# Kernel tuning notes

Hardware: AMD Instinct MI355X
Metric: run time of the kernel (lower is better)

Reference implementation:

```python
import jax, jax.numpy as jnp
import numpy as np

HEAD_SIZE = 16  # matches init_kwargs head_size


def _rope_angles(seq_len, half_dim, base=10000.0):
    # standard RoPE frequencies, matches typical precompute_pos_cis
    freqs = 1.0 / (base ** (np.arange(0, half_dim, dtype=np.float32) / half_dim))
    t = np.arange(seq_len, dtype=np.float32)
    ang = np.outer(t, freqs)  # (S, half_dim)
    return jnp.asarray(np.cos(ang)), jnp.asarray(np.sin(ang))


def setup_inputs() -> dict:
    key = jax.random.key(0)
    ks = jax.random.split(key, 10)
    B, S, D = 2, 2048, 1024
    hd = D // HEAD_SIZE
    pos_cos, pos_sin = _rope_angles(S, hd // 2)
    w = lambda k: jax.random.normal(k, (D, D), jnp.float32) * 0.02
    b = lambda k: jax.random.normal(k, (D,), jnp.float32) * 0.02
    return {
        "x": jax.random.normal(ks[0], (B, S, D), jnp.float32),
        "pos_cos": pos_cos,
        "pos_sin": pos_sin,
        "wq_w": w(ks[1]), "wq_b": b(ks[2]),
        "wk_w": w(ks[3]), "wk_b": b(ks[4]),
        "wv_w": w(ks[5]), "wv_b": b(ks[6]),
        "wo_w": w(ks[7]), "wo_b": b(ks[8]),
    }


def _apply_rope(t, cos, sin):
    # t: (B, S, H, hd); cos/sin: (S, hd//2) -> broadcast (1, S, 1, hd//2)
    B, S, H, hd = t.shape
    tr = t.reshape(B, S, H, hd // 2, 2)
    a, b = tr[..., 0], tr[..., 1]
    c = cos[None, :, None, :]
    s = sin[None, :, None, :]
    # complex multiply (a + ib) * (c + is)
    out_r = a * c - b * s
    out_i = a * s + b * c
    return jnp.stack([out_r, out_i], axis=-1).reshape(B, S, H, hd)


def reference(x, pos_cos, pos_sin, wq_w, wq_b, wk_w, wk_b, wv_w, wv_b, wo_w, wo_b):
    B, S, D = x.shape
    H = HEAD_SIZE
    hd = D // H
    q = (x @ wq_w.T + wq_b).reshape(B, S, H, hd)
    k = (x @ wk_w.T + wk_b).reshape(B, S, H, hd)
    v = (x @ wv_w.T + wv_b).reshape(B, S, H, hd)
    q = _apply_rope(q, pos_cos, pos_sin)
    k = _apply_rope(k, pos_cos, pos_sin)
    scale = 1.0 / jnp.sqrt(jnp.asarray(hd, x.dtype))
    scores = jnp.einsum('bshd,bthd->bhst', q, k) * scale  # (B,H,S,S)
    causal = jnp.tril(jnp.ones((S, S), bool))
    scores = jnp.where(causal[None, None], scores, jnp.asarray(-jnp.inf, scores.dtype))
    probs = jax.nn.softmax(scores, axis=-1)
    out = jnp.einsum('bhst,bthd->bshd', probs, v).reshape(B, S, D)
    return out @ wo_w.T + wo_b
```

## Files before the change

### kernel.cpp

```cpp
#include <hip/hip_runtime.h>
#include <stdint.h>
#include <stddef.h>


typedef __bf16 bf16x8 __attribute__((ext_vector_type(8)));
typedef float  f32x4  __attribute__((ext_vector_type(4)));

__device__ __forceinline__ unsigned short f2b(float f) {
  union { float f; uint32_t u; } v; v.f = f;
  uint32_t u = v.u;
  return (unsigned short)((u + 0x7FFFu + ((u >> 16) & 1u)) >> 16);
}

__device__ __forceinline__ void async16(const void* g, void* l) {
  __builtin_amdgcn_global_load_lds(
      (const __attribute__((address_space(1))) void*)g,
      (__attribute__((address_space(3))) void*)l, 16, 0, 0);
}

__global__ void cast_kernel(const float* __restrict__ in,
                            unsigned short* __restrict__ out, int n4) {
  int i = blockIdx.x * blockDim.x + threadIdx.x;
  if (i >= n4) return;
  float4 v = ((const float4*)in)[i];
  ushort4 o;
  o.x = f2b(v.x); o.y = f2b(v.y); o.z = f2b(v.z); o.w = f2b(v.w);
  ((ushort4*)out)[i] = o;
}

__global__ void cast_w_kernel(const float* __restrict__ wq, const float* __restrict__ wk,
                              const float* __restrict__ wv, const float* __restrict__ wo,
                              unsigned short* __restrict__ wqkv,
                              unsigned short* __restrict__ wobf) {
  int i = blockIdx.x * blockDim.x + threadIdx.x;
  const int sel = i >> 18, k = i & ((1 << 18) - 1);
  const float* src = (sel == 0) ? wq : (sel == 1) ? wk : (sel == 2) ? wv : wo;
  float4 v = ((const float4*)src)[k];
  ushort4 o;
  o.x = f2b(v.x); o.y = f2b(v.y); o.z = f2b(v.z); o.w = f2b(v.w);
  if (sel < 3) ((ushort4*)wqkv)[(size_t)sel * 262144 + k] = o;
  else         ((ushort4*)wobf)[k] = o;
}

__global__ __launch_bounds__(256) void qkv_gemm_kernel(
    const unsigned short* __restrict__ A,
    const unsigned short* __restrict__ W,
    const float* __restrict__ biasq, const float* __restrict__ biask,
    const float* __restrict__ biasv,
    const float* __restrict__ cp, const float* __restrict__ sp,
    unsigned short* __restrict__ qo,
    unsigned short* __restrict__ ko,
    unsigned short* __restrict__ vo)
{
  __shared__ unsigned short As[128 * 64];
  __shared__ unsigned short Bs[128 * 64];
  const int tid  = threadIdx.x;
  const int w    = tid >> 6, l = tid & 63;
  const int lm   = l & 15,  quad = l >> 4;
  const int nblk = blockIdx.x;
  const int m0   = blockIdx.y * 128;
  const int n0g  = nblk * 128;
  const int wm   = (w >> 1) * 64, wn = (w & 1) * 64;

  const f32x4 fzero = {0.f, 0.f, 0.f, 0.f};
  f32x4 acc[4][4];
#pragma unroll
  for (int i = 0; i < 4; ++i)
#pragma unroll
    for (int j = 0; j < 4; ++j) acc[i][j] = fzero;

  for (int k0 = 0; k0 < 1024; k0 += 64) {
    __syncthreads();
#pragma unroll
    for (int q = 0; q < 4; ++q) {
      const int row = w * 16 + lm + (q & 1) * 64;
      const int kc  = quad + (q >> 1) * 4;
      const size_t ldsb = ((size_t)(w + 4 * (q & 1)) * 128 + 64 * (q >> 1)) * 8;
      async16(A + (size_t)(m0 + row) * 1024 + k0 + kc * 8, As + ldsb);
      async16(W + (size_t)(n0g + row) * 1024 + k0 + kc * 8, Bs + ldsb);
    }
    __syncthreads();
#pragma unroll
    for (int kk = 0; kk < 2; ++kk) {
      bf16x8 af[4], bfc[4];
#pragma unroll
      for (int i = 0; i < 4; ++i)
        af[i] = *(const bf16x8*)(As + (size_t)((((w >> 1) * 4 + i) * 128 + kk * 64 + l)) * 8);
#pragma unroll
      for (int j = 0; j < 4; ++j)
        bfc[j] = *(const bf16x8*)(Bs + (size_t)((((w & 1) * 4 + j) * 128 + kk * 64 + l)) * 8);
#pragma unroll
      for (int i = 0; i < 4; ++i)
#pragma unroll
        for (int j = 0; j < 4; ++j)
          acc[i][j] = __builtin_amdgcn_mfma_f32_16x16x32_bf16(af[i], bfc[j], acc[i][j], 0, 0, 0);
    }
  }

  const int which = nblk >> 3;
  const int n0    = (nblk & 7) * 128;
  const float* bias = (which == 0) ? biasq : (which == 1) ? biask : biasv;
#pragma unroll
  for (int i = 0; i < 4; ++i) {
#pragma unroll
    for (int j = 0; j < 4; ++j) {
      const int n = n0 + wn + j * 16 + lm;
      const float bval = bias[n];
      const int h = n >> 6, d = n & 63;
      float vals[4];
#pragma unroll
      for (int r = 0; r < 4; ++r) {
        const int m = m0 + wm + i * 16 + quad * 4 + r;
        const int srow = m & 2047;
        float val = acc[i][j][r] + bval;
        if (which != 2) {
          const float c  = cp[srow * 32 + (d >> 1)];
          const float sn = sp[srow * 32 + (d >> 1)];
          const float part = __shfl_xor(val, 1, 64);
          val = (d & 1) ? (part * sn + val * c) : (val * c - part * sn);
        }
        vals[r] = val;
      }
      const int mbase = m0 + wm + i * 16 + quad * 4;
      const int b = mbase >> 11, s0 = mbase & 2047;
      const int bh = (b << 4) + h;
      if (which == 0) {
#pragma unroll
        for (int r = 0; r < 4; ++r)
          qo[((size_t)bh * 2048 + s0 + r) * 64 + d] = f2b(vals[r]);
      } else if (which == 1) {
#pragma unroll
        for (int r = 0; r < 4; ++r) {
          const int s = s0 + r;
          ko[((size_t)bh * 32 + (s >> 6)) * 4096 +
             (size_t)(((d >> 3) * 64 + (s & 63))) * 8 + (d & 7)] = f2b(vals[r]);
        }
      } else {
        uint32_t w0 = (uint32_t)f2b(vals[0]) | ((uint32_t)f2b(vals[1]) << 16);
        uint32_t w1 = (uint32_t)f2b(vals[2]) | ((uint32_t)f2b(vals[3]) << 16);
        uint2 pk; pk.x = w0; pk.y = w1;
        *(uint2*)(vo + ((size_t)bh * 32 + (s0 >> 6)) * 4096 +
                  (size_t)((((s0 & 63) >> 3) * 64 + d)) * 8 + (s0 & 7)) = pk;
      }
    }
  }
}

__global__ __launch_bounds__(256, 4) void flash_kernel(
    const unsigned short* __restrict__ Q,
    const unsigned short* __restrict__ K,
    const unsigned short* __restrict__ VT,
    unsigned short* __restrict__ O)
{
  constexpr int PSTRIDE = 72;
  __shared__ unsigned short Ps[64 * PSTRIDE];
  const int tid = threadIdx.x;
  const int w = tid >> 6, l = tid & 63, lm = l & 15, quad = l >> 4;
  const int bh = blockIdx.x, qt = 31 - (int)blockIdx.y;
  const int row0 = qt * 64 + w * 16;

  bf16x8 aq[2];
#pragma unroll
  for (int kc = 0; kc < 2; ++kc)
    aq[kc] = *(const bf16x8*)(Q + ((size_t)bh * 2048 + row0 + lm) * 64 + kc * 32 + quad * 8);

  const f32x4 fzero = {0.f, 0.f, 0.f, 0.f};
  f32x4 Oacc[4];
#pragma unroll
  for (int jo = 0; jo < 4; ++jo) Oacc[jo] = fzero;
  float m_i = -1e30f, l_i = 0.f;

  const int nkv = qt + 1;

#pragma unroll 1
  for (int kt = 0; kt < nkv - 1; ++kt) {
    const size_t tbase = ((size_t)bh * 32 + kt) * 4096;
    bf16x8 kf[2][4], vf[2][4];
#pragma unroll
    for (int kc = 0; kc < 2; ++kc)
#pragma unroll
      for (int tb = 0; tb < 4; ++tb) {
        const size_t off = tbase + (size_t)(((kc * 4 + quad) * 64 + tb * 16 + lm)) * 8;
        kf[kc][tb] = *(const bf16x8*)(K + off);
        vf[kc][tb] = *(const bf16x8*)(VT + off);
      }
    f32x4 Sc[4];
#pragma unroll
    for (int tb = 0; tb < 4; ++tb) Sc[tb] = fzero;
#pragma unroll
    for (int kc = 0; kc < 2; ++kc)
#pragma unroll
      for (int tb = 0; tb < 4; ++tb)
        Sc[tb] = __builtin_amdgcn_mfma_f32_16x16x32_bf16(kf[kc][tb], aq[kc], Sc[tb], 0, 0, 0);

    float mx = -1e30f;
#pragma unroll
    for (int tb = 0; tb < 4; ++tb)
#pragma unroll
      for (int r = 0; r < 4; ++r) {
        float s = Sc[tb][r] * 0.125f;
        Sc[tb][r] = s;
        mx = fmaxf(mx, s);
      }
    mx = fmaxf(mx, __shfl_xor(mx, 16, 64));
    mx = fmaxf(mx, __shfl_xor(mx, 32, 64));

    const bool skip = (bool)__all(mx - m_i <= 8.0f);
    float alpha = 1.f;
    if (!skip) {
      const float mnew = fmaxf(m_i, mx);
      alpha = __expf(m_i - mnew);
      m_i = mnew;
    }
    const float mref = m_i;

    float ps = 0.f;
#pragma unroll
    for (int tb = 0; tb < 4; ++tb) {
      float p0 = __expf(Sc[tb][0] - mref), p1 = __expf(Sc[tb][1] - mref);
      float p2 = __expf(Sc[tb][2] - mref), p3 = __expf(Sc[tb][3] - mref);
      ps += (p0 + p1) + (p2 + p3);
      uint2 pk;
      pk.x = (uint32_t)f2b(p0) | ((uint32_t)f2b(p1) << 16);
      pk.y = (uint32_t)f2b(p2) | ((uint32_t)f2b(p3) << 16);
      *(uint2*)(Ps + (size_t)(w * 16 + lm) * PSTRIDE + tb * 16 + quad * 4) = pk;
    }
    ps += __shfl_xor(ps, 16, 64);
    ps += __shfl_xor(ps, 32, 64);
    if (skip) {
      l_i += ps;
    } else {
      l_i = l_i * alpha + ps;
      float af4[4];
#pragma unroll
      for (int r = 0; r < 4; ++r) af4[r] = __shfl(alpha, quad * 4 + r, 64);
#pragma unroll
      for (int jo = 0; jo < 4; ++jo)
#pragma unroll
        for (int r = 0; r < 4; ++r) Oacc[jo][r] *= af4[r];
    }

#pragma unroll
    for (int kc = 0; kc < 2; ++kc) {
      bf16x8 ap = *(const bf16x8*)(Ps + (size_t)(w * 16 + lm) * PSTRIDE + kc * 32 + quad * 8);
#pragma unroll
      for (int jo = 0; jo < 4; ++jo)
        Oacc[jo] = __builtin_amdgcn_mfma_f32_16x16x32_bf16(ap, vf[kc][jo], Oacc[jo], 0, 0, 0);
    }
  }

  {
    const size_t tbase = ((size_t)bh * 32 + qt) * 4096;
    bf16x8 kf[2][4], vf[2][4];
#pragma unroll
    for (int kc = 0; kc < 2; ++kc)
#pragma unroll
      for (int tb = 0; tb < 4; ++tb) {
        const size_t off = tbase + (size_t)(((kc * 4 + quad) * 64 + tb * 16 + lm)) * 8;
        kf[kc][tb] = *(const bf16x8*)(K + off);
        vf[kc][tb] = *(const bf16x8*)(VT + off);
      }
    f32x4 Sc[4];
#pragma unroll
    for (int tb = 0; tb < 4; ++tb) Sc[tb] = fzero;
#pragma unroll
    for (int kc = 0; kc < 2; ++kc)
#pragma unroll
      for (int tb = 0; tb < 4; ++tb)
        Sc[tb] = __builtin_amdgcn_mfma_f32_16x16x32_bf16(kf[kc][tb], aq[kc], Sc[tb], 0, 0, 0);

    const int mrel = w * 16 + lm;
    float mx = -1e30f;
#pragma unroll
    for (int tb = 0; tb < 4; ++tb)
#pragma unroll
      for (int r = 0; r < 4; ++r) {
        float s = Sc[tb][r] * 0.125f;
        if (tb * 16 + quad * 4 + r > mrel) s = -1e30f;
        Sc[tb][r] = s;
        mx = fmaxf(mx, s);
      }
    mx = fmaxf(mx, __shfl_xor(mx, 16, 64));
    mx = fmaxf(mx, __shfl_xor(mx, 32, 64));
    const float mnew  = fmaxf(m_i, mx);
    const float alpha = __expf(m_i - mnew);
    m_i = mnew;

    float ps = 0.f;
#pragma unroll
    for (int tb = 0; tb < 4; ++tb) {
      float p0 = __expf(Sc[tb][0] - mnew), p1 = __expf(Sc[tb][1] - mnew);
      float p2 = __expf(Sc[tb][2] - mnew), p3 = __expf(Sc[tb][3] - mnew);
      ps += (p0 + p1) + (p2 + p3);
      uint2 pk;
      pk.x = (uint32_t)f2b(p0) | ((uint32_t)f2b(p1) << 16);
      pk.y = (uint32_t)f2b(p2) | ((uint32_t)f2b(p3) << 16);
      *(uint2*)(Ps + (size_t)(w * 16 + lm) * PSTRIDE + tb * 16 + quad * 4) = pk;
    }
    ps += __shfl_xor(ps, 16, 64);
    ps += __shfl_xor(ps, 32, 64);
    l_i = l_i * alpha + ps;

    float af4[4];
#pragma unroll
    for (int r = 0; r < 4; ++r) af4[r] = __shfl(alpha, quad * 4 + r, 64);
#pragma unroll
    for (int jo = 0; jo < 4; ++jo)
#pragma unroll
      for (int r = 0; r < 4; ++r) Oacc[jo][r] *= af4[r];

#pragma unroll
    for (int kc = 0; kc < 2; ++kc) {
      bf16x8 ap = *(const bf16x8*)(Ps + (size_t)(w * 16 + lm) * PSTRIDE + kc * 32 + quad * 8);
#pragma unroll
      for (int jo = 0; jo < 4; ++jo)
        Oacc[jo] = __builtin_amdgcn_mfma_f32_16x16x32_bf16(ap, vf[kc][jo], Oacc[jo], 0, 0, 0);
    }
  }

  float lf[4];
#pragma unroll
  for (int r = 0; r < 4; ++r) lf[r] = 1.0f / __shfl(l_i, quad * 4 + r, 64);
  const int b = bh >> 4, h = bh & 15;
#pragma unroll
  for (int jo = 0; jo < 4; ++jo)
#pragma unroll
    for (int r = 0; r < 4; ++r) {
      const int s   = row0 + quad * 4 + r;
      const int col = h * 64 + jo * 16 + lm;
      O[((size_t)b * 2048 + s) * 1024 + col] = f2b(Oacc[jo][r] * lf[r]);
    }
}

__global__ __launch_bounds__(256) void oproj_gemm_kernel(
    const unsigned short* __restrict__ A,
    const unsigned short* __restrict__ W,
    const float* __restrict__ bias,
    float* __restrict__ out)
{
  __shared__ unsigned short As[64 * 64];
  __shared__ unsigned short Bs[128 * 64];
  const int tid = threadIdx.x;
  const int w = tid >> 6, l = tid & 63;
  const int lm = l & 15, quad = l >> 4;
  const int m0 = blockIdx.y * 64;
  const int n0 = blockIdx.x * 128;

  const f32x4 fzero = {0.f, 0.f, 0.f, 0.f};
  f32x4 acc[4][2];
#pragma unroll
  for (int i = 0; i < 4; ++i)
#pragma unroll
    for (int j = 0; j < 2; ++j) acc[i][j] = fzero;

  for (int k0 = 0; k0 < 1024; k0 += 64) {
    __syncthreads();
#pragma unroll
    for (int q = 0; q < 2; ++q) {
      const int row = w * 16 + lm;
      const int kc  = quad + 4 * q;
      async16(A + (size_t)(m0 + row) * 1024 + k0 + kc * 8,
              As + ((size_t)w * 128 + 64 * q) * 8);
    }
#pragma unroll
    for (int q = 0; q < 4; ++q) {
      const int row = w * 16 + lm + (q & 1) * 64;
      const int kc  = quad + 4 * (q >> 1);
      async16(W + (size_t)(n0 + row) * 1024 + k0 + kc * 8,
              Bs + ((size_t)(w + 4 * (q & 1)) * 128 + 64 * (q >> 1)) * 8);
    }
    __syncthreads();
#pragma unroll
    for (int kk = 0; kk < 2; ++kk) {
      bf16x8 af[4], bfc[2];
#pragma unroll
      for (int i = 0; i < 4; ++i)
        af[i] = *(const bf16x8*)(As + (size_t)((i * 128 + kk * 64 + l)) * 8);
#pragma unroll
      for (int j = 0; j < 2; ++j)
        bfc[j] = *(const bf16x8*)(Bs + (size_t)(((w * 2 + j) * 128 + kk * 64 + l)) * 8);
#pragma unroll
      for (int i = 0; i < 4; ++i)
#pragma unroll
        for (int j = 0; j < 2; ++j)
          acc[i][j] = __builtin_amdgcn_mfma_f32_16x16x32_bf16(af[i], bfc[j], acc[i][j], 0, 0, 0);
    }
  }

#pragma unroll
  for (int i = 0; i < 4; ++i) {
#pragma unroll
    for (int j = 0; j < 2; ++j) {
      const int n = n0 + w * 32 + j * 16 + lm;
      const float bval = bias[n];
#pragma unroll
      for (int r = 0; r < 4; ++r) {
        const int m = m0 + i * 16 + quad * 4 + r;
        out[(size_t)m * 1024 + n] = acc[i][j][r] + bval;
      }
    }
  }
}

extern "C" void kernel_launch(void* const* d_in, const int* in_sizes, int n_in,
                              void* d_out, int out_size, void* d_ws, size_t ws_size,
                              hipStream_t stream) {
  (void)in_sizes; (void)n_in; (void)out_size; (void)ws_size;
  const float* x  = (const float*)d_in[0];
  const float* cp = (const float*)d_in[1];
  const float* sp = (const float*)d_in[2];
  const float* wq = (const float*)d_in[3];
  const float* bq = (const float*)d_in[4];
  const float* wk = (const float*)d_in[5];
  const float* bk = (const float*)d_in[6];
  const float* wv = (const float*)d_in[7];
  const float* bv = (const float*)d_in[8];
  const float* wo = (const float*)d_in[9];
  const float* bo = (const float*)d_in[10];
  float* out = (float*)d_out;

  unsigned short* xbf  = (unsigned short*)d_ws;
  unsigned short* wqkv = xbf  + (size_t)4 * 1024 * 1024;
  unsigned short* wobf = wqkv + (size_t)3 * 1024 * 1024;
  unsigned short* qbf  = wobf + (size_t)1 * 1024 * 1024;
  unsigned short* kbf  = qbf  + (size_t)4 * 1024 * 1024;
  unsigned short* vbf  = kbf  + (size_t)4 * 1024 * 1024;
  unsigned short* obf  = vbf  + (size_t)4 * 1024 * 1024;

  hipLaunchKernelGGL(cast_kernel, dim3(4096), dim3(256), 0, stream, x, xbf, 1048576);
  hipLaunchKernelGGL(cast_w_kernel, dim3(4096), dim3(256), 0, stream,
                     wq, wk, wv, wo, wqkv, wobf);

  hipLaunchKernelGGL(qkv_gemm_kernel, dim3(24, 32), dim3(256), 0, stream,
                     xbf, wqkv, bq, bk, bv, cp, sp, qbf, kbf, vbf);
  hipLaunchKernelGGL(flash_kernel, dim3(32, 32), dim3(256), 0, stream,
                     qbf, kbf, vbf, obf);
  hipLaunchKernelGGL(oproj_gemm_kernel, dim3(8, 64), dim3(256), 0, stream,
                     obf, wobf, bo, out);
}
```

Baseline: 226.7 us.

## Pre-tile QKV GEMM operands in cast kernels and read fragments directly from global

```diff
diff --git a/kernel.cpp b/kernel.cpp
--- a/kernel.cpp
+++ b/kernel.cpp
@@ -16,6 +16,47 @@
   __builtin_amdgcn_global_load_lds(
       (const __attribute__((address_space(1))) void*)g,
       (__attribute__((address_space(3))) void*)l, 16, 0, 0);
+}
+
+__global__ void cast_x_tiled_kernel(const float* __restrict__ in,
+                                    unsigned short* __restrict__ out) {
+  int i = blockIdx.x * blockDim.x + threadIdx.x;
+  const int L  = i & 1023;
+  const int kt = (i >> 10) & 15;
+  const int pn = i >> 14;
+  const int row = pn * 128 + ((L >> 7) << 4) + (L & 15);
+  const int k0  = kt * 64 + ((L >> 4) & 7) * 8;
+  const float4* src = (const float4*)(in + (size_t)row * 1024 + k0);
+  float4 a = src[0], b = src[1];
+  uint4 pk;
+  pk.x = (uint32_t)f2b(a.x) | ((uint32_t)f2b(a.y) << 16);
+  pk.y = (uint32_t)f2b(a.z) | ((uint32_t)f2b(a.w) << 16);
+  pk.z = (uint32_t)f2b(b.x) | ((uint32_t)f2b(b.y) << 16);
+  pk.w = (uint32_t)f2b(b.z) | ((uint32_t)f2b(b.w) << 16);
+  *(uint4*)(out + (size_t)i * 8) = pk;
+}
+
+__global__ void cast_w_tiled_kernel(const float* __restrict__ wq,
+                                    const float* __restrict__ wk,
+                                    const float* __restrict__ wv,
+                                    unsigned short* __restrict__ out) {
+  int i = blockIdx.x * blockDim.x + threadIdx.x;
+  const int mat = i >> 17;
+  const int rem = i & 131071;
+  const int L  = rem & 1023;
+  const int kt = (rem >> 10) & 15;
+  const int pn = rem >> 14;
+  const float* src = (mat == 0) ? wq : (mat == 1) ? wk : wv;
+  const int row = pn * 128 + ((L >> 7) << 4) + (L & 15);
+  const int k0  = kt * 64 + ((L >> 4) & 7) * 8;
+  const float4* s = (const float4*)(src + (size_t)row * 1024 + k0);
+  float4 a = s[0], b = s[1];
+  uint4 pk;
+  pk.x = (uint32_t)f2b(a.x) | ((uint32_t)f2b(a.y) << 16);
+  pk.y = (uint32_t)f2b(a.z) | ((uint32_t)f2b(a.w) << 16);
+  pk.z = (uint32_t)f2b(b.x) | ((uint32_t)f2b(b.y) << 16);
+  pk.w = (uint32_t)f2b(b.z) | ((uint32_t)f2b(b.w) << 16);
+  *(uint4*)(out + (size_t)i * 8) = pk;
 }
 
 __global__ void cast_kernel(const float* __restrict__ in,
@@ -28,21 +69,7 @@
   ((ushort4*)out)[i] = o;
 }
 
-__global__ void cast_w_kernel(const float* __restrict__ wq, const float* __restrict__ wk,
-                              const float* __restrict__ wv, const float* __restrict__ wo,
-                              unsigned short* __restrict__ wqkv,
-                              unsigned short* __restrict__ wobf) {
-  int i = blockIdx.x * blockDim.x + threadIdx.x;
-  const int sel = i >> 18, k = i & ((1 << 18) - 1);
-  const float* src = (sel == 0) ? wq : (sel == 1) ? wk : (sel == 2) ? wv : wo;
-  float4 v = ((const float4*)src)[k];
-  ushort4 o;
-  o.x = f2b(v.x); o.y = f2b(v.y); o.z = f2b(v.z); o.w = f2b(v.w);
-  if (sel < 3) ((ushort4*)wqkv)[(size_t)sel * 262144 + k] = o;
-  else         ((ushort4*)wobf)[k] = o;
-}
-
-__global__ __launch_bounds__(256) void qkv_gemm_kernel(
+__global__ __launch_bounds__(256, 4) void qkv_gemm_kernel(
     const unsigned short* __restrict__ A,
     const unsigned short* __restrict__ W,
     const float* __restrict__ biasq, const float* __restrict__ biask,
@@ -52,15 +79,15 @@
     unsigned short* __restrict__ ko,
     unsigned short* __restrict__ vo)
 {
-  __shared__ unsigned short As[128 * 64];
-  __shared__ unsigned short Bs[128 * 64];
   const int tid  = threadIdx.x;
   const int w    = tid >> 6, l = tid & 63;
   const int lm   = l & 15,  quad = l >> 4;
   const int nblk = blockIdx.x;
   const int m0   = blockIdx.y * 128;
-  const int n0g  = nblk * 128;
   const int wm   = (w >> 1) * 64, wn = (w & 1) * 64;
+
+  const unsigned short* At = A + (size_t)blockIdx.y * 16 * 8192;
+  const unsigned short* Wt = W + (size_t)nblk * 16 * 8192;
 
   const f32x4 fzero = {0.f, 0.f, 0.f, 0.f};
   f32x4 acc[4][4];
@@ -69,26 +96,19 @@
 #pragma unroll
     for (int j = 0; j < 4; ++j) acc[i][j] = fzero;
 
-  for (int k0 = 0; k0 < 1024; k0 += 64) {
-    __syncthreads();
-#pragma unroll
-    for (int q = 0; q < 4; ++q) {
-      const int row = w * 16 + lm + (q & 1) * 64;
-      const int kc  = quad + (q >> 1) * 4;
-      const size_t ldsb = ((size_t)(w + 4 * (q & 1)) * 128 + 64 * (q >> 1)) * 8;
-      async16(A + (size_t)(m0 + row) * 1024 + k0 + kc * 8, As + ldsb);
-      async16(W + (size_t)(n0g + row) * 1024 + k0 + kc * 8, Bs + ldsb);
-    }
-    __syncthreads();
+#pragma unroll 1
+  for (int t = 0; t < 16; ++t) {
+    const unsigned short* Ab = At + (size_t)t * 8192;
+    const unsigned short* Wb = Wt + (size_t)t * 8192;
 #pragma unroll
     for (int kk = 0; kk < 2; ++kk) {
       bf16x8 af[4], bfc[4];
 #pragma unroll
       for (int i = 0; i < 4; ++i)
-        af[i] = *(const bf16x8*)(As + (size_t)((((w >> 1) * 4 + i) * 128 + kk * 64 + l)) * 8);
+        af[i] = *(const bf16x8*)(Ab + (size_t)((((w >> 1) * 4 + i) * 128 + kk * 64 + l)) * 8);
 #pragma unroll
       for (int j = 0; j < 4; ++j)
-        bfc[j] = *(const bf16x8*)(Bs + (size_t)((((w & 1) * 4 + j) * 128 + kk * 64 + l)) * 8);
+        bfc[j] = *(const bf16x8*)(Wb + (size_t)((((w & 1) * 4 + j) * 128 + kk * 64 + l)) * 8);
 #pragma unroll
       for (int i = 0; i < 4; ++i)
 #pragma unroll
@@ -427,9 +447,10 @@
   unsigned short* vbf  = kbf  + (size_t)4 * 1024 * 1024;
   unsigned short* obf  = vbf  + (size_t)4 * 1024 * 1024;
 
-  hipLaunchKernelGGL(cast_kernel, dim3(4096), dim3(256), 0, stream, x, xbf, 1048576);
-  hipLaunchKernelGGL(cast_w_kernel, dim3(4096), dim3(256), 0, stream,
-                     wq, wk, wv, wo, wqkv, wobf);
+  hipLaunchKernelGGL(cast_x_tiled_kernel, dim3(2048), dim3(256), 0, stream, x, xbf);
+  hipLaunchKernelGGL(cast_w_tiled_kernel, dim3(1536), dim3(256), 0, stream,
+                     wq, wk, wv, wqkv);
+  hipLaunchKernelGGL(cast_kernel, dim3(1024), dim3(256), 0, stream, wo, wobf, 262144);
 
   hipLaunchKernelGGL(qkv_gemm_kernel, dim3(24, 32), dim3(256), 0, stream,
                      xbf, wqkv, bq, bk, bv, cp, sp, qbf, kbf, vbf);
```

Measured after the change: 223.9 us. Within noise of the previous version (-1.2%).
